# Optimization experiments

Hardware: AMD Instinct MI355X
Metric: run time of the kernel (lower is better)

Reference implementation:

```python
import jax, jax.numpy as jnp
import numpy as np

N_ATOMS = 128
BATCH = 512


def _build_buffers(n):
    # Segments: all non-adjacent bond pairs (i,i+1,j,j+1), j >= i+2, j+1 <= n-1.
    segs = np.array([(i, i + 1, j, j + 1)
                     for i in range(n - 3)
                     for j in range(i + 2, n - 1)], dtype=np.int32)  # (S,4)

    def pidx(a, b):  # linear index of pair (a,b), a<b, in row-major triu(offset=1) order
        return a * n - a * (a + 1) // 2 + (b - a - 1)

    # Each writhe value scatters into its 4 incident residue pairs.
    # Pairs (0,1) [triu idx 0] and (n-2,n-1) [last triu idx] are never incident,
    # so ranks among interior pairs are (triu idx - 1); they are re-inserted by pad.
    inc = []
    for (i, _, j, _) in segs:
        for (a, b) in ((i, j), (i, j + 1), (i + 1, j), (i + 1, j + 1)):
            inc.append(pidx(a, b) - 1)
    indices = np.array(inc, dtype=np.int32)  # (4*S,)

    # Sort permutation placing [upper-triu values, lower-triu values] into
    # row-major order of all off-diagonal (r,c) entries, keyed by r*n + c.
    iu = np.stack(np.triu_indices(n, 1))  # (2, P) row-major
    vals = np.concatenate([iu[0] * n + iu[1], iu[1] * n + iu[0]])
    sort = np.argsort(vals).astype(np.int32)  # (n^2 - n,)
    return segs, indices, sort


def setup_inputs() -> dict:
    key = jax.random.key(0)
    xyz = jax.random.normal(key, (BATCH, N_ATOMS, 3), dtype=jnp.float32)
    segs, indices, sort = _build_buffers(N_ATOMS)
    return {
        "xyz": xyz,
        "segments": jnp.asarray(segs),
        "indices": jnp.asarray(indices),
        "sort": jnp.asarray(sort),
    }


def _divnorm(x):
    return x / jnp.linalg.norm(x, axis=-1, keepdims=True)


def _writhe(xyz, segments):
    # xyz: (B,N,3); segments: (S,4) -> writhe per segment pair, (B,S)
    B, S = xyz.shape[0], segments.shape[0]
    p = xyz[:, segments]  # (B,S,4,3) gathered endpoints [s1a,s1b,s2a,s2b]
    # d[k] = normalize(p_{2+j} - p_i), k = 2*i + j  (the 4 inter-segment directions)
    d = _divnorm((p[:, :, None, 2:, :] - p[:, :, :2, None, :]).reshape(B, S, 4, 3))
    axial = jnp.cross(p[:, :, 3] - p[:, :, 2], p[:, :, 1] - p[:, :, 0])  # (B,S,3)
    signs = jnp.sign(jnp.sum(axial * d[:, :, 0], -1))  # (B,S)
    # 4 face normals of the spherical quadrilateral, then Gauss-Bonnet angle sum
    nrm = _divnorm(jnp.cross(d[:, :, jnp.array([0, 1, 3, 2])],
                             d[:, :, jnp.array([1, 3, 2, 0])]))  # (B,S,4,3)
    cosang = jnp.clip(jnp.sum(nrm * nrm[:, :, jnp.array([1, 2, 3, 0])], -1), -1.0, 1.0)
    omega = jnp.arcsin(cosang).sum(-1)  # (B,S)
    return omega * signs / (2.0 * jnp.pi)


def _laplacian(wr, indices, sort, n):
    # wr: (B,S); scatter-add each writhe into its 4 incident residue pairs,
    # pad back the two untouched pairs, symmetrize, and sort into row-major
    # off-diagonal order -> (B, n^2 - n)
    M = (n * n - n) // 2 - 2
    triu = jnp.zeros((wr.shape[0], M), wr.dtype).at[:, indices].add(
        jnp.repeat(wr, 4, axis=1))
    padded = jnp.pad(triu, ((0, 0), (1, 1)))
    return jnp.concatenate([padded, padded], axis=1)[:, sort]


def reference(xyz, segments, indices, sort):
    xyz = xyz.reshape(-1, N_ATOMS, 3)
    wr = _writhe(xyz, segments)
    return _laplacian(wr, indices, sort, N_ATOMS)
```

## Files before the change

kernel.cpp:

```cpp
#include <hip/hip_runtime.h>
#include <math.h>

#define NATOMS    128
#define NSEG      7875
#define NSEG_PAD  8192
#define NPAIR     8128
#define OUT_PER_B 16256
#define BLOCK     1024

typedef float v2f __attribute__((ext_vector_type(2)));
__device__ __forceinline__ v2f mk2(float a, float b) { v2f r; r.x = a; r.y = b; return r; }

struct P3 { v2f x, y, z; };
__device__ __forceinline__ P3 psub(P3 a, P3 b) { return {a.x - b.x, a.y - b.y, a.z - b.z}; }
__device__ __forceinline__ P3 pcross(P3 a, P3 b) {
    return {a.y * b.z - a.z * b.y, a.z * b.x - a.x * b.z, a.x * b.y - a.y * b.x};
}
__device__ __forceinline__ v2f pdot(P3 a, P3 b) { return a.x * b.x + a.y * b.y + a.z * b.z; }
__device__ __forceinline__ v2f prsq(v2f q) {
    v2f r; r.x = __builtin_amdgcn_rsqf(q.x); r.y = __builtin_amdgcn_rsqf(q.y); return r;
}
__device__ __forceinline__ v2f pclip1(v2f x) {
    return __builtin_elementwise_min(__builtin_elementwise_max(x, mk2(-1.f, -1.f)),
                                     mk2(1.f, 1.f));
}

__device__ __forceinline__ v2f fast_asin2(v2f x) {
    v2f a = __builtin_elementwise_abs(x);
    v2f p = mk2(-0.0187293f, -0.0187293f);
    p = p * a + mk2( 0.0742610f,  0.0742610f);
    p = p * a + mk2(-0.2121144f, -0.2121144f);
    p = p * a + mk2( 1.5707288f,  1.5707288f);
    v2f om = mk2(1.0f, 1.0f) - a;
    v2f sq; sq.x = __builtin_amdgcn_sqrtf(om.x); sq.y = __builtin_amdgcn_sqrtf(om.y);
    v2f r = mk2(1.57079632679f, 1.57079632679f) - sq * p;
    return __builtin_elementwise_copysign(r, x);
}

__device__ __forceinline__ int seg_row_base(int i) { return 125 * i - (__umul24(i, i - 1) >> 1); }
__device__ __forceinline__ int pair_row_base(int a) { return (__umul24(a, 255 - a) >> 1); }

__device__ __forceinline__ v2f seg_writhe_pair(unsigned pa, unsigned pb,
                                               const float* sx, const float* sy,
                                               const float* sz) {
    int jA = (int)(pa & 127u), iA = (int)(pa >> 7);
    int jB = (int)(pb & 127u), iB = (int)(pb >> 7);

    P3 p0 = {mk2(sx[iA],     sx[iB]),     mk2(sy[iA],     sy[iB]),     mk2(sz[iA],     sz[iB])};
    P3 p1 = {mk2(sx[iA + 1], sx[iB + 1]), mk2(sy[iA + 1], sy[iB + 1]), mk2(sz[iA + 1], sz[iB + 1])};
    P3 p2 = {mk2(sx[jA],     sx[jB]),     mk2(sy[jA],     sy[jB]),     mk2(sz[jA],     sz[jB])};
    P3 p3 = {mk2(sx[jA + 1], sx[jB + 1]), mk2(sy[jA + 1], sy[jB + 1]), mk2(sz[jA + 1], sz[jB + 1])};

    P3 u0 = psub(p2, p0);
    P3 u1 = psub(p3, p0);
    P3 u2 = psub(p2, p1);
    P3 u3 = psub(p3, p1);

    P3 n0 = pcross(u0, u1);
    P3 n1 = pcross(u1, u3);
    P3 n2 = pcross(u3, u2);
    P3 n3 = pcross(u2, u0);

    v2f q0 = pdot(n0, n0);
    v2f q1 = pdot(n1, n1);
    v2f q2 = pdot(n2, n2);
    v2f q3 = pdot(n3, n3);

    v2f c0 = pclip1(pdot(n0, n1) * prsq(q0 * q1));
    v2f c1 = pclip1(pdot(n1, n2) * prsq(q1 * q2));
    v2f c2 = pclip1(pdot(n2, n3) * prsq(q2 * q3));
    v2f c3 = pclip1(pdot(n3, n0) * prsq(q3 * q0));

    v2f sd = pdot(n2, u0);
    v2f omega = fast_asin2(c0) + fast_asin2(c1) + fast_asin2(c2) + fast_asin2(c3);

    v2f sgn;
    sgn.x = (sd.x > 0.f) ? -1.f : ((sd.x < 0.f) ? 1.f : 0.f);
    sgn.y = (sd.y > 0.f) ? -1.f : ((sd.y < 0.f) ? 1.f : 0.f);

    return omega * sgn * mk2(0.15915494309189535f, 0.15915494309189535f);
}

__global__ __launch_bounds__(BLOCK, 8) void writhe_fused(
    const float* __restrict__ xyz,
    float*       __restrict__ out)
{
    __shared__ float sx[NATOMS], sy[NATOMS], sz[NATOMS];
    __shared__ float swr[NSEG_PAD];
    __shared__ unsigned short sidx[NSEG_PAD];
    __shared__ unsigned short spair[NPAIR];

    const int b = blockIdx.x;
    const int t = threadIdx.x;

    if (t < 3 * NATOMS) {
        float v = xyz[(size_t)b * (3 * NATOMS) + t];
        int a = t / 3, c = t - 3 * a;
        if (c == 0) sx[a] = v; else if (c == 1) sy[a] = v; else sz[a] = v;
    }

    {
        int s = t * 8;
        if (s < NSEG) {
            int i = (int)((251.0f - __builtin_amdgcn_sqrtf(63001.0f - 8.0f * (float)s)) * 0.5f);
            i = max(i, 0);
            i += (seg_row_base(i + 1) <= s);
            i += (seg_row_base(i + 1) <= s);
            i -= (seg_row_base(i) > s);
            i -= (seg_row_base(i) > s);
            int j = s - seg_row_base(i) + i + 2;
            #pragma unroll
            for (int k = 0; k < 8; ++k) {
                if (s < NSEG) sidx[s] = (unsigned short)((i << 7) | j);
                ++s; ++j;
                if (j > 126) { ++i; j = i + 2; }
            }
        }
        if (t < NSEG_PAD - NSEG) sidx[NSEG + t] = (unsigned short)((124 << 7) | 126);
    }
    {
        int p = t * 8;
        if (p < NPAIR) {
            int a = (int)((255.0f - __builtin_amdgcn_sqrtf(65025.0f - 8.0f * (float)p)) * 0.5f);
            a = max(a, 0);
            a += (pair_row_base(a + 1) <= p);
            a += (pair_row_base(a + 1) <= p);
            a -= (pair_row_base(a) > p);
            a -= (pair_row_base(a) > p);
            int bb = a + 1 + (p - pair_row_base(a));
            #pragma unroll
            for (int k = 0; k < 8; ++k) {
                if (p < NPAIR) spair[p] = (unsigned short)((a << 7) | bb);
                ++p; ++bb;
                if (bb > 127) { ++a; bb = a + 1; }
            }
        }
    }
    __syncthreads();

    #pragma unroll
    for (int g = 0; g < 2; ++g) {
        const int sA = g * 4096 + t;
        v2f w1 = seg_writhe_pair(sidx[sA],        sidx[sA + 1024], sx, sy, sz);
        v2f w2 = seg_writhe_pair(sidx[sA + 2048], sidx[sA + 3072], sx, sy, sz);
        swr[sA]        = w1.x;
        swr[sA + 1024] = w1.y;
        swr[sA + 2048] = w2.x;
        swr[sA + 3072] = w2.y;
    }
    __syncthreads();

    float* ob = out + (size_t)b * OUT_PER_B;
    for (int p = t; p < NPAIR; p += BLOCK) {
        unsigned pk = spair[p];
        int bb = (int)(pk & 127u);
        int a  = (int)(pk >> 7);

        int am1 = a - 1;
        int s00 = 125 * am1 - ((am1 * (am1 - 1)) >> 1) + bb - a - 2;
        int s10 = s00 + 125 - a;

        bool v00 = (a >= 1) && (a <= 125) && (bb >= a + 2);
        bool v01 = (a >= 1) && (a <= 125) && (bb <= 126);
        bool v10 = (a <= 124) && (bb >= a + 3);
        bool v11 = (a <= 124) && (bb <= 126) && (bb >= a + 2);

        int c00 = min(max(s00,     0), NSEG - 1);
        int c01 = min(max(s00 + 1, 0), NSEG - 1);
        int c10 = min(max(s10,     0), NSEG - 1);
        int c11 = min(max(s10 + 1, 0), NSEG - 1);

        float sum = (v00 ? swr[c00] : 0.0f) + (v01 ? swr[c01] : 0.0f)
                  + (v10 ? swr[c10] : 0.0f) + (v11 ? swr[c11] : 0.0f);

        int k1 = 127 * a + bb - 1;
        int k2 = 127 * bb + a;
        ob[k1] = sum;
        ob[k2] = sum;
    }
}

extern "C" void kernel_launch(void* const* d_in, const int* in_sizes, int n_in,
                              void* d_out, int out_size, void* d_ws, size_t ws_size,
                              hipStream_t stream) {
    const float* xyz = (const float*)d_in[0];
    float*       out = (float*)d_out;

    int B = in_sizes[0] / (NATOMS * 3);
    writhe_fused<<<B, BLOCK, 0, stream>>>(xyz, out);
}
```

Baseline: 92.75 us.

## Compute adjacent segment pairs (j, j+1) together to share endpoint differences

Each thread now handles two consecutive segment pairs that share the first bond i and adjacent second bonds j and j+1. The shared endpoint differences and the common cross product between them are computed once, and only five atoms are loaded from LDS per pair instead of eight. The index table shrinks to half-size entries for even j-i offsets, with a clamp and a guard covering the last column. The aim is to cut ALU and LDS load work in the writhe stage, at the cost of extra index arithmetic and scattered stores into swr.

```diff
diff --git a/kernel.cpp b/kernel.cpp
--- a/kernel.cpp
+++ b/kernel.cpp
@@ -4,6 +4,8 @@
 #define NATOMS    128
 #define NSEG      7875
 #define NSEG_PAD  8192
+#define NPAIRSEG  3969
+#define NPAIR_PAD 4096
 #define NPAIR     8128
 #define OUT_PER_B 16256
 #define BLOCK     1024
@@ -12,7 +14,6 @@
 __device__ __forceinline__ v2f mk2(float a, float b) { v2f r; r.x = a; r.y = b; return r; }
 
 struct P3 { v2f x, y, z; };
-__device__ __forceinline__ P3 psub(P3 a, P3 b) { return {a.x - b.x, a.y - b.y, a.z - b.z}; }
 __device__ __forceinline__ P3 pcross(P3 a, P3 b) {
     return {a.y * b.z - a.z * b.y, a.z * b.x - a.x * b.z, a.x * b.y - a.y * b.x};
 }
@@ -40,21 +41,26 @@
 __device__ __forceinline__ int seg_row_base(int i) { return 125 * i - (__umul24(i, i - 1) >> 1); }
 __device__ __forceinline__ int pair_row_base(int a) { return (__umul24(a, 255 - a) >> 1); }
 
-__device__ __forceinline__ v2f seg_writhe_pair(unsigned pa, unsigned pb,
-                                               const float* sx, const float* sy,
-                                               const float* sz) {
-    int jA = (int)(pa & 127u), iA = (int)(pa >> 7);
-    int jB = (int)(pb & 127u), iB = (int)(pb >> 7);
-
-    P3 p0 = {mk2(sx[iA],     sx[iB]),     mk2(sy[iA],     sy[iB]),     mk2(sz[iA],     sz[iB])};
-    P3 p1 = {mk2(sx[iA + 1], sx[iB + 1]), mk2(sy[iA + 1], sy[iB + 1]), mk2(sz[iA + 1], sz[iB + 1])};
-    P3 p2 = {mk2(sx[jA],     sx[jB]),     mk2(sy[jA],     sy[jB]),     mk2(sz[jA],     sz[jB])};
-    P3 p3 = {mk2(sx[jA + 1], sx[jB + 1]), mk2(sy[jA + 1], sy[jB + 1]), mk2(sz[jA + 1], sz[jB + 1])};
-
-    P3 u0 = psub(p2, p0);
-    P3 u1 = psub(p3, p0);
-    P3 u2 = psub(p2, p1);
-    P3 u3 = psub(p3, p1);
+__device__ __forceinline__ v2f writhe_pair_j(int i, int j, const float* sx,
+                                             const float* sy, const float* sz) {
+    int jc2 = min(j + 2, 127);
+    float pix = sx[i],     piy = sy[i],     piz = sz[i];
+    float qix = sx[i + 1], qiy = sy[i + 1], qiz = sz[i + 1];
+    float P0x = sx[j],     P0y = sy[j],     P0z = sz[j];
+    float P1x = sx[j + 1], P1y = sy[j + 1], P1z = sz[j + 1];
+    float P2x = sx[jc2],   P2y = sy[jc2],   P2z = sz[jc2];
+
+    float a0x = P0x - pix, a0y = P0y - piy, a0z = P0z - piz;
+    float a1x = P1x - pix, a1y = P1y - piy, a1z = P1z - piz;
+    float a2x = P2x - pix, a2y = P2y - piy, a2z = P2z - piz;
+    float b0x = P0x - qix, b0y = P0y - qiy, b0z = P0z - qiz;
+    float b1x = P1x - qix, b1y = P1y - qiy, b1z = P1z - qiz;
+    float b2x = P2x - qix, b2y = P2y - qiy, b2z = P2z - qiz;
+
+    P3 u0 = {mk2(a0x, a1x), mk2(a0y, a1y), mk2(a0z, a1z)};
+    P3 u1 = {mk2(a1x, a2x), mk2(a1y, a2y), mk2(a1z, a2z)};
+    P3 u2 = {mk2(b0x, b1x), mk2(b0y, b1y), mk2(b0z, b1z)};
+    P3 u3 = {mk2(b1x, b2x), mk2(b1y, b2y), mk2(b1z, b2z)};
 
     P3 n0 = pcross(u0, u1);
     P3 n1 = pcross(u1, u3);
@@ -87,7 +93,7 @@
 {
     __shared__ float sx[NATOMS], sy[NATOMS], sz[NATOMS];
     __shared__ float swr[NSEG_PAD];
-    __shared__ unsigned short sidx[NSEG_PAD];
+    __shared__ unsigned short tpair[NPAIR_PAD];
     __shared__ unsigned short spair[NPAIR];
 
     const int b = blockIdx.x;
@@ -111,12 +117,15 @@
             int j = s - seg_row_base(i) + i + 2;
             #pragma unroll
             for (int k = 0; k < 8; ++k) {
-                if (s < NSEG) sidx[s] = (unsigned short)((i << 7) | j);
+                if (s < NSEG && (((j - i) & 1) == 0)) {
+                    int q = 63 * i - (__umul24(i, i) >> 2) + ((j - i - 2) >> 1);
+                    tpair[q] = (unsigned short)((i << 7) | j);
+                }
                 ++s; ++j;
                 if (j > 126) { ++i; j = i + 2; }
             }
         }
-        if (t < NSEG_PAD - NSEG) sidx[NSEG + t] = (unsigned short)((124 << 7) | 126);
+        if (t < NPAIR_PAD - NPAIRSEG) tpair[NPAIRSEG + t] = (unsigned short)((124 << 7) | 126);
     }
     {
         int p = t * 8;
@@ -140,13 +149,21 @@
 
     #pragma unroll
     for (int g = 0; g < 2; ++g) {
-        const int sA = g * 4096 + t;
-        v2f w1 = seg_writhe_pair(sidx[sA],        sidx[sA + 1024], sx, sy, sz);
-        v2f w2 = seg_writhe_pair(sidx[sA + 2048], sidx[sA + 3072], sx, sy, sz);
-        swr[sA]        = w1.x;
-        swr[sA + 1024] = w1.y;
-        swr[sA + 2048] = w2.x;
-        swr[sA + 3072] = w2.y;
+        int e1 = g * 2048 + t;
+        int e2 = e1 + 1024;
+        unsigned k1 = tpair[e1], k2 = tpair[e2];
+        int j1 = (int)(k1 & 127u), i1 = (int)(k1 >> 7);
+        int j2 = (int)(k2 & 127u), i2 = (int)(k2 >> 7);
+
+        v2f w1 = writhe_pair_j(i1, j1, sx, sy, sz);
+        v2f w2 = writhe_pair_j(i2, j2, sx, sy, sz);
+
+        int s1 = seg_row_base(i1) + j1 - i1 - 2;
+        int s2 = seg_row_base(i2) + j2 - i2 - 2;
+        swr[s1] = w1.x;
+        if (j1 < 126) swr[s1 + 1] = w1.y;
+        swr[s2] = w2.x;
+        if (j2 < 126) swr[s2 + 1] = w2.y;
     }
     __syncthreads();
 
```

New measurement: 93.70 us. Within noise of the previous version (+1.0%).
